# Kernel tuning notes

Hardware: AMD Instinct MI355X
Metric: run time of the kernel (lower is better)

Reference implementation:

```python
import jax, jax.numpy as jnp
import numpy as np

D_IN, D_BIAS, H, DH = 256, 128, 8, 32

def _layernorm(x, w, b, eps=1e-5):
    mu = jnp.mean(x, axis=-1, keepdims=True)
    var = jnp.var(x, axis=-1, keepdims=True)
    return (x - mu) * jax.lax.rsqrt(var + eps) * w + b

def setup_inputs() -> dict:
    key = jax.random.key(0)
    ks = jax.random.split(key, 8)
    B, L = 1, 768
    x = jax.random.normal(ks[0], (B, L, D_IN), dtype=jnp.float32)
    bias = jax.random.normal(ks[1], (B, L, L, D_BIAS), dtype=jnp.float32)
    s_in = 1.0 / np.sqrt(D_IN)
    s_b = 1.0 / np.sqrt(D_BIAS)
    return {
        "x": x,
        "bias": bias,
        "ln_in_w": jnp.ones((D_IN,), jnp.float32),
        "ln_in_b": jnp.zeros((D_IN,), jnp.float32),
        "ln_b_w": jnp.ones((D_BIAS,), jnp.float32),
        "ln_b_b": jnp.zeros((D_BIAS,), jnp.float32),
        "Wq": jax.random.normal(ks[2], (D_IN, H * DH), jnp.float32) * s_in,
        "Wk": jax.random.normal(ks[3], (D_IN, H * DH), jnp.float32) * s_in,
        "Wv": jax.random.normal(ks[4], (D_IN, H * DH), jnp.float32) * s_in,
        "Wb": jax.random.normal(ks[5], (D_BIAS, H), jnp.float32) * s_b,
        "Wg": jax.random.normal(ks[6], (D_IN, H * DH), jnp.float32) * 0.02,
        "bg": jnp.ones((H * DH,), jnp.float32),
        "Wo": jax.random.normal(ks[7], (H * DH, D_IN), jnp.float32) * 0.02,
        "bo": jnp.zeros((D_IN,), jnp.float32),
    }

def reference(x, bias, ln_in_w, ln_in_b, ln_b_w, ln_b_b, Wq, Wk, Wv, Wb, Wg, bg, Wo, bo):
    B, L, _ = x.shape
    scaling = 1.0 / np.sqrt(DH)
    xn = _layernorm(x, ln_in_w, ln_in_b)            # (B,L,D_IN)
    bn = _layernorm(bias, ln_b_w, ln_b_b)           # (B,L,L,D_BIAS)
    q = (xn @ Wq).reshape(B, L, H, DH)
    k = (xn @ Wk).reshape(B, L, H, DH) * scaling
    v = (xn @ Wv).reshape(B, L, H, DH)
    b = bn @ Wb                                     # (B,L,L,H)
    gate = jax.nn.sigmoid(xn @ Wg + bg)             # (B,L,H*DH)
    attn = jnp.einsum('bqhd,bkhd->bqkh', q, k) + b  # (B,q,k,h)
    attn = jax.nn.softmax(attn, axis=2)             # softmax over key dim
    out = jnp.einsum('bqkh,bkhd->bqhd', attn, v).reshape(B, L, H * DH)
    out = gate * out
    return out @ Wo + bo
```

## Files before the change

### kernel.cpp

```cpp
#include <hip/hip_runtime.h>

#define LQ 768
#define DIN 256
#define DB 128
#define NH 8
#define DH 32

#define OFF_QB 0
#define OFF_KT (LQ*DIN)
#define OFF_VB (2*LQ*DIN)
#define OFF_GB (3*LQ*DIN)
#define OFF_W2 (4*LQ*DIN)
#define OFF_SC (OFF_W2 + DB*NH)
#define OFF_LG (OFF_SC + 16)

__global__ __launch_bounds__(128) void setup_kernel(
    const float* __restrict__ lbw, const float* __restrict__ lbb,
    const float* __restrict__ Wb, float* __restrict__ W2, float* __restrict__ SC)
{
    const int d = threadIdx.x;
    const int lane = d & 63, wv = d >> 6;
    float w = lbw[d], b = lbb[d];
    float pS[NH], pC[NH];
    #pragma unroll
    for (int h = 0; h < NH; h++) {
        float wb = Wb[d*NH + h];
        float w2 = w * wb;
        W2[d*NH + h] = w2;
        pS[h] = w2;
        pC[h] = b * wb;
    }
    #pragma unroll
    for (int m = 1; m <= 32; m <<= 1) {
        #pragma unroll
        for (int h = 0; h < NH; h++) { pS[h] += __shfl_xor(pS[h], m); pC[h] += __shfl_xor(pC[h], m); }
    }
    __shared__ float red[2][16];
    if (lane == 0) {
        #pragma unroll
        for (int h = 0; h < NH; h++) { red[wv][h] = pS[h]; red[wv][NH+h] = pC[h]; }
    }
    __syncthreads();
    if (d < 16) SC[d] = red[0][d] + red[1][d];
}

__global__ __launch_bounds__(256) void proj_kernel(
    const float* __restrict__ x, const float* __restrict__ lnw, const float* __restrict__ lnb,
    const float* __restrict__ Wq, const float* __restrict__ Wk, const float* __restrict__ Wv,
    const float* __restrict__ Wg, const float* __restrict__ bg,
    float* __restrict__ qb, float* __restrict__ kT, float* __restrict__ vb, float* __restrict__ gb)
{
    const int tid = threadIdx.x;
    const int lane = tid & 63, rr = tid >> 6;
    const int row = blockIdx.x * 4 + rr;
    __shared__ float xn[4][DIN];

    float4 xv = ((const float4*)x)[row * (DIN/4) + lane];
    float s  = xv.x + xv.y + xv.z + xv.w;
    float ss = xv.x*xv.x + xv.y*xv.y + xv.z*xv.z + xv.w*xv.w;
    #pragma unroll
    for (int m = 1; m <= 32; m <<= 1) { s += __shfl_xor(s, m); ss += __shfl_xor(ss, m); }
    float mu  = s * (1.0f/DIN);
    float inv = rsqrtf(ss * (1.0f/DIN) - mu*mu + 1e-5f);
    float4 wv4 = ((const float4*)lnw)[lane];
    float4 bv4 = ((const float4*)lnb)[lane];
    float4 r4;
    r4.x = (xv.x - mu)*inv*wv4.x + bv4.x;
    r4.y = (xv.y - mu)*inv*wv4.y + bv4.y;
    r4.z = (xv.z - mu)*inv*wv4.z + bv4.z;
    r4.w = (xv.w - mu)*inv*wv4.w + bv4.w;
    *((float4*)&xn[rr][lane*4]) = r4;
    __syncthreads();

    const int col = tid;
    float aq[4] = {0,0,0,0}, ak[4] = {0,0,0,0}, av[4] = {0,0,0,0}, ag[4] = {0,0,0,0};
    for (int i4 = 0; i4 < DIN/4; i4++) {
        float4 x0 = *((const float4*)&xn[0][i4*4]);
        float4 x1 = *((const float4*)&xn[1][i4*4]);
        float4 x2 = *((const float4*)&xn[2][i4*4]);
        float4 x3 = *((const float4*)&xn[3][i4*4]);
        const float* p0 = (const float*)&x0;
        const float* p1 = (const float*)&x1;
        const float* p2 = (const float*)&x2;
        const float* p3 = (const float*)&x3;
        #pragma unroll
        for (int e = 0; e < 4; e++) {
            const int i = i4*4 + e;
            float wq = Wq[i*DIN + col], wk = Wk[i*DIN + col];
            float wvv = Wv[i*DIN + col], wg = Wg[i*DIN + col];
            aq[0] = fmaf(p0[e], wq, aq[0]); aq[1] = fmaf(p1[e], wq, aq[1]);
            aq[2] = fmaf(p2[e], wq, aq[2]); aq[3] = fmaf(p3[e], wq, aq[3]);
            ak[0] = fmaf(p0[e], wk, ak[0]); ak[1] = fmaf(p1[e], wk, ak[1]);
            ak[2] = fmaf(p2[e], wk, ak[2]); ak[3] = fmaf(p3[e], wk, ak[3]);
            av[0] = fmaf(p0[e], wvv, av[0]); av[1] = fmaf(p1[e], wvv, av[1]);
            av[2] = fmaf(p2[e], wvv, av[2]); av[3] = fmaf(p3[e], wvv, av[3]);
            ag[0] = fmaf(p0[e], wg, ag[0]); ag[1] = fmaf(p1[e], wg, ag[1]);
            ag[2] = fmaf(p2[e], wg, ag[2]); ag[3] = fmaf(p3[e], wg, ag[3]);
        }
    }
    const float kscale = 0.17677669529663687f;
    float bgv = bg[col];
    #pragma unroll
    for (int r = 0; r < 4; r++) {
        const int orow = blockIdx.x*4 + r;
        qb[orow*DIN + col] = aq[r];
        vb[orow*DIN + col] = av[r];
        gb[orow*DIN + col] = 1.0f/(1.0f + __expf(-(ag[r] + bgv)));
    }
    *((float4*)&kT[col*LQ + blockIdx.x*4]) =
        make_float4(ak[0]*kscale, ak[1]*kscale, ak[2]*kscale, ak[3]*kscale);
}

__global__ __launch_bounds__(128) void bias_kernel(
    const float* __restrict__ bias, const float* __restrict__ W2g,
    const float* __restrict__ SCg, float* __restrict__ logits)
{
    __shared__ float tile[2][64 * 129];
    const int tid  = threadIdx.x;
    const int w    = tid >> 6;
    const int lane = tid & 63;
    const int wid  = blockIdx.x * 2 + w;

    float* tw = &tile[w][0];
    const int wbase = (lane >> 5) * 129 + (lane & 31) * 4;
    const int rbase = lane * 129;

    float Sh[NH], Ch[NH];
    #pragma unroll
    for (int h = 0; h < NH; h++) { Sh[h] = SCg[h]; Ch[h] = SCg[NH + h]; }

    float4 v[32];

    const int tau0 = wid * 9;

    {
        const int q  = tau0 / 12;
        const int kb = (tau0 % 12) * 64;
        const float4* gs = (const float4*)(bias + ((size_t)q * LQ + kb) * DB);
        #pragma unroll
        for (int c = 0; c < 32; c++) v[c] = gs[c * 64 + lane];
        #pragma unroll
        for (int c = 0; c < 32; c++) {
            tw[wbase + c*258 + 0] = v[c].x;
            tw[wbase + c*258 + 1] = v[c].y;
            tw[wbase + c*258 + 2] = v[c].z;
            tw[wbase + c*258 + 3] = v[c].w;
        }
    }

    for (int t = 0; t < 9; t++) {
        const int tau = tau0 + t;

        if (t + 1 < 9) {
            const int qn  = (tau + 1) / 12;
            const int kbn = ((tau + 1) % 12) * 64;
            const float4* gs = (const float4*)(bias + ((size_t)qn * LQ + kbn) * DB);
            #pragma unroll
            for (int c = 0; c < 32; c++) v[c] = gs[c * 64 + lane];
        }
        asm volatile("" ::: "memory");

        float s = 0.f, ss = 0.f;
        float acc[NH] = {0,0,0,0,0,0,0,0};
        #pragma unroll 4
        for (int d = 0; d < DB; d++) {
            float xv = tw[rbase + d];
            const float* wr = W2g + d * NH;
            s += xv; ss = fmaf(xv, xv, ss);
            #pragma unroll
            for (int h = 0; h < NH; h++) acc[h] = fmaf(xv, wr[h], acc[h]);
        }

        {
            const int q  = tau / 12;
            const int kb = (tau % 12) * 64;
            float mu  = s * (1.0f/DB);
            float inv = rsqrtf(ss * (1.0f/DB) - mu*mu + 1e-5f);
            float lo[NH];
            #pragma unroll
            for (int h = 0; h < NH; h++)
                lo[h] = fmaf(inv, fmaf(-mu, Sh[h], acc[h]), Ch[h]);
            float4* dst = (float4*)(logits + ((size_t)q*LQ + kb + lane)*NH);
            dst[0] = make_float4(lo[0], lo[1], lo[2], lo[3]);
            dst[1] = make_float4(lo[4], lo[5], lo[6], lo[7]);
        }

        if (t + 1 < 9) {
            #pragma unroll
            for (int c = 0; c < 32; c++) {
                tw[wbase + c*258 + 0] = v[c].x;
                tw[wbase + c*258 + 1] = v[c].y;
                tw[wbase + c*258 + 2] = v[c].z;
                tw[wbase + c*258 + 3] = v[c].w;
            }
        }
    }
}

__global__ __launch_bounds__(256) void attn_kernel(
    const float* __restrict__ logits, const float* __restrict__ qbuf,
    const float* __restrict__ kT, const float* __restrict__ vbuf,
    const float* __restrict__ gb, const float* __restrict__ Wo,
    const float* __restrict__ bo, float* __restrict__ out)
{
    const int tid = threadIdx.x;
    const int q0 = blockIdx.x * 2;
    __shared__ float pT[2][NH][776];
    __shared__ float ao[2][DIN];
    __shared__ float isum[2][NH];

    #pragma unroll
    for (int r = 0; r < 2; r++) {
        const float4* rp = (const float4*)(logits + (size_t)(q0 + r)*LQ*NH);
        #pragma unroll
        for (int ii = 0; ii < 6; ii++) {
            int jj = ii*256 + tid;
            float4 t = rp[jj];
            int k = jj >> 1, h0 = (jj & 1) << 2;
            pT[r][h0+0][k] = t.x; pT[r][h0+1][k] = t.y;
            pT[r][h0+2][k] = t.z; pT[r][h0+3][k] = t.w;
        }
    }
    __syncthreads();

    if (tid < 192) {
        const float* q0p = qbuf + (size_t)q0*DIN;
        const float* q1p = q0p + DIN;
        #pragma unroll
        for (int h = 0; h < NH; h++) {
            float a00=0,a01=0,a02=0,a03=0, a10=0,a11=0,a12=0,a13=0;
            #pragma unroll
            for (int dd = 0; dd < DH; dd++) {
                const int d = h*DH + dd;
                float4 kv = *(const float4*)(kT + (size_t)d*LQ + tid*4);
                float qa = q0p[d], qc = q1p[d];
                a00 = fmaf(qa, kv.x, a00); a01 = fmaf(qa, kv.y, a01);
                a02 = fmaf(qa, kv.z, a02); a03 = fmaf(qa, kv.w, a03);
                a10 = fmaf(qc, kv.x, a10); a11 = fmaf(qc, kv.y, a11);
                a12 = fmaf(qc, kv.z, a12); a13 = fmaf(qc, kv.w, a13);
            }
            float4 p0 = *(float4*)&pT[0][h][tid*4];
            p0.x += a00; p0.y += a01; p0.z += a02; p0.w += a03;
            *(float4*)&pT[0][h][tid*4] = p0;
            float4 p1 = *(float4*)&pT[1][h][tid*4];
            p1.x += a10; p1.y += a11; p1.z += a12; p1.w += a13;
            *(float4*)&pT[1][h][tid*4] = p1;
        }
    }
    __syncthreads();

    {
        const int r = tid >> 7, h = (tid >> 4) & 7, l = tid & 15;
        float4* row = (float4*)&pT[r][h][0];
        float m = -1e30f;
        for (int i = l; i < 192; i += 16) {
            float4 v = row[i];
            m = fmaxf(m, fmaxf(fmaxf(v.x, v.y), fmaxf(v.z, v.w)));
        }
        #pragma unroll
        for (int mm = 1; mm <= 8; mm <<= 1) m = fmaxf(m, __shfl_xor(m, mm));
        float sum = 0.f;
        for (int i = l; i < 192; i += 16) {
            float4 v = row[i];
            v.x = __expf(v.x - m); v.y = __expf(v.y - m);
            v.z = __expf(v.z - m); v.w = __expf(v.w - m);
            sum += v.x + v.y + v.z + v.w;
            row[i] = v;
        }
        #pragma unroll
        for (int mm = 1; mm <= 8; mm <<= 1) sum += __shfl_xor(sum, mm);
        if (l == 0) isum[r][h] = 1.0f / sum;
    }
    __syncthreads();

    {
        const int h = tid >> 5, d = tid & 31;
        const float* vp = vbuf + h*DH + d;
        const float4* p0r = (const float4*)&pT[0][h][0];
        const float4* p1r = (const float4*)&pT[1][h][0];
        float a0 = 0.f, a1 = 0.f;
        for (int k4 = 0; k4 < 192; k4++) {
            float4 p0 = p0r[k4], p1 = p1r[k4];
            float v0 = vp[(size_t)(k4*4+0)*DIN];
            float v1 = vp[(size_t)(k4*4+1)*DIN];
            float v2 = vp[(size_t)(k4*4+2)*DIN];
            float v3 = vp[(size_t)(k4*4+3)*DIN];
            a0 = fmaf(p0.x, v0, a0); a0 = fmaf(p0.y, v1, a0);
            a0 = fmaf(p0.z, v2, a0); a0 = fmaf(p0.w, v3, a0);
            a1 = fmaf(p1.x, v0, a1); a1 = fmaf(p1.y, v1, a1);
            a1 = fmaf(p1.z, v2, a1); a1 = fmaf(p1.w, v3, a1);
        }
        ao[0][tid] = a0 * isum[0][h] * gb[(q0+0)*DIN + tid];
        ao[1][tid] = a1 * isum[1][h] * gb[(q0+1)*DIN + tid];
    }
    __syncthreads();

    {
        const int col = tid;
        float o0 = bo[col], o1 = o0;
        for (int i = 0; i < DIN; i++) {
            float wv = Wo[i*DIN + col];
            o0 = fmaf(ao[0][i], wv, o0);
            o1 = fmaf(ao[1][i], wv, o1);
        }
        out[(q0+0)*DIN + col] = o0;
        out[(q0+1)*DIN + col] = o1;
    }
}

extern "C" void kernel_launch(void* const* d_in, const int* in_sizes, int n_in,
                              void* d_out, int out_size, void* d_ws, size_t ws_size,
                              hipStream_t stream) {
    const float* x    = (const float*)d_in[0];
    const float* bias = (const float*)d_in[1];
    const float* lnw  = (const float*)d_in[2];
    const float* lnb  = (const float*)d_in[3];
    const float* lbw  = (const float*)d_in[4];
    const float* lbb  = (const float*)d_in[5];
    const float* Wq   = (const float*)d_in[6];
    const float* Wk   = (const float*)d_in[7];
    const float* Wv   = (const float*)d_in[8];
    const float* Wb   = (const float*)d_in[9];
    const float* Wg   = (const float*)d_in[10];
    const float* bg   = (const float*)d_in[11];
    const float* Wo   = (const float*)d_in[12];
    const float* bo   = (const float*)d_in[13];

    float* ws = (float*)d_ws;
    float* qb = ws + OFF_QB;
    float* kT = ws + OFF_KT;
    float* vb = ws + OFF_VB;
    float* gb = ws + OFF_GB;
    float* W2 = ws + OFF_W2;
    float* SC = ws + OFF_SC;
    float* lg = ws + OFF_LG;

    setup_kernel<<<1, 128, 0, stream>>>(lbw, lbb, Wb, W2, SC);
    proj_kernel<<<LQ/4, 256, 0, stream>>>(x, lnw, lnb, Wq, Wk, Wv, Wg, bg, qb, kT, vb, gb);
    bias_kernel<<<512, 128, 0, stream>>>(bias, W2, SC, lg);
    attn_kernel<<<LQ/2, 256, 0, stream>>>(lg, qb, kT, vb, gb, Wo, bo, (float*)d_out);
}
```

Baseline: 164.0 us.

## Precompute QK scores in a tiled kernel and fuse them into the bias-logit pass

Moves the per-head Q·K dot products out of the attention kernel into a separate shared-memory tiled qk kernel that writes a full L×L×H score buffer. The bias kernel is rewritten to one thread per (q,key) pair, reading the bias row directly instead of staging it through an LDS transpose, and adds the precomputed scores into the logits. The setup kernel is merged into the projection launch as an extra block, and K is stored row-major instead of transposed. In exchange this adds an extra ~19MB write and read of the QK buffer, and each thread's strided 512-byte bias reads may coalesce less well.

```diff
diff --git a/kernel.cpp b/kernel.cpp
--- a/kernel.cpp
+++ b/kernel.cpp
@@ -7,50 +7,53 @@
 #define DH 32
 
 #define OFF_QB 0
-#define OFF_KT (LQ*DIN)
+#define OFF_KB (LQ*DIN)
 #define OFF_VB (2*LQ*DIN)
 #define OFF_GB (3*LQ*DIN)
 #define OFF_W2 (4*LQ*DIN)
 #define OFF_SC (OFF_W2 + DB*NH)
-#define OFF_LG (OFF_SC + 16)
-
-__global__ __launch_bounds__(128) void setup_kernel(
-    const float* __restrict__ lbw, const float* __restrict__ lbb,
-    const float* __restrict__ Wb, float* __restrict__ W2, float* __restrict__ SC)
-{
-    const int d = threadIdx.x;
-    const int lane = d & 63, wv = d >> 6;
-    float w = lbw[d], b = lbb[d];
-    float pS[NH], pC[NH];
-    #pragma unroll
-    for (int h = 0; h < NH; h++) {
-        float wb = Wb[d*NH + h];
-        float w2 = w * wb;
-        W2[d*NH + h] = w2;
-        pS[h] = w2;
-        pC[h] = b * wb;
-    }
-    #pragma unroll
-    for (int m = 1; m <= 32; m <<= 1) {
-        #pragma unroll
-        for (int h = 0; h < NH; h++) { pS[h] += __shfl_xor(pS[h], m); pC[h] += __shfl_xor(pC[h], m); }
-    }
-    __shared__ float red[2][16];
-    if (lane == 0) {
-        #pragma unroll
-        for (int h = 0; h < NH; h++) { red[wv][h] = pS[h]; red[wv][NH+h] = pC[h]; }
-    }
-    __syncthreads();
-    if (d < 16) SC[d] = red[0][d] + red[1][d];
-}
-
-__global__ __launch_bounds__(256) void proj_kernel(
+#define OFF_QK (OFF_SC + 16)
+#define OFF_LG (OFF_QK + LQ*LQ*NH)
+
+__global__ __launch_bounds__(256) void projsetup_kernel(
     const float* __restrict__ x, const float* __restrict__ lnw, const float* __restrict__ lnb,
     const float* __restrict__ Wq, const float* __restrict__ Wk, const float* __restrict__ Wv,
     const float* __restrict__ Wg, const float* __restrict__ bg,
-    float* __restrict__ qb, float* __restrict__ kT, float* __restrict__ vb, float* __restrict__ gb)
+    const float* __restrict__ lbw, const float* __restrict__ lbb, const float* __restrict__ Wb,
+    float* __restrict__ qb, float* __restrict__ kb, float* __restrict__ vb, float* __restrict__ gb,
+    float* __restrict__ W2, float* __restrict__ SC)
 {
     const int tid = threadIdx.x;
+
+    if (blockIdx.x == 192) {
+        if (tid < 128) {
+            const int d = tid, lane = d & 63, wv = d >> 6;
+            float w = lbw[d], b = lbb[d];
+            float pS[NH], pC[NH];
+            #pragma unroll
+            for (int h = 0; h < NH; h++) {
+                float wb = Wb[d*NH + h];
+                float w2 = w * wb;
+                W2[d*NH + h] = w2;
+                pS[h] = w2;
+                pC[h] = b * wb;
+            }
+            #pragma unroll
+            for (int m = 1; m <= 32; m <<= 1) {
+                #pragma unroll
+                for (int h = 0; h < NH; h++) { pS[h] += __shfl_xor(pS[h], m); pC[h] += __shfl_xor(pC[h], m); }
+            }
+            __shared__ float red[2][16];
+            if (lane == 0) {
+                #pragma unroll
+                for (int h = 0; h < NH; h++) { red[wv][h] = pS[h]; red[wv][NH+h] = pC[h]; }
+            }
+            __syncthreads();
+            if (d < 16) SC[d] = red[0][d] + red[1][d];
+        }
+        return;
+    }
+
     const int lane = tid & 63, rr = tid >> 6;
     const int row = blockIdx.x * 4 + rr;
     __shared__ float xn[4][DIN];
@@ -104,102 +107,139 @@
     for (int r = 0; r < 4; r++) {
         const int orow = blockIdx.x*4 + r;
         qb[orow*DIN + col] = aq[r];
+        kb[orow*DIN + col] = ak[r] * kscale;
         vb[orow*DIN + col] = av[r];
         gb[orow*DIN + col] = 1.0f/(1.0f + __expf(-(ag[r] + bgv)));
     }
-    *((float4*)&kT[col*LQ + blockIdx.x*4]) =
-        make_float4(ak[0]*kscale, ak[1]*kscale, ak[2]*kscale, ak[3]*kscale);
-}
-
-__global__ __launch_bounds__(128) void bias_kernel(
+}
+
+__global__ __launch_bounds__(256) void qk_kernel(
+    const float* __restrict__ qb, const float* __restrict__ kb, float* __restrict__ qkT)
+{
+    __shared__ float q_l[32*260];
+    __shared__ float k_l[32*260];
+    const int tid = threadIdx.x;
+    const int bq = blockIdx.x, bk = blockIdx.y;
+
+    {
+        const int row = tid >> 3, cg = tid & 7;
+        const float4* qs = (const float4*)(qb + (size_t)(bq*32 + row)*DIN + cg*32);
+        const float4* ks = (const float4*)(kb + (size_t)(bk*32 + row)*DIN + cg*32);
+        #pragma unroll
+        for (int j = 0; j < 8; j++) {
+            *(float4*)&q_l[row*260 + cg*32 + j*4] = qs[j];
+            *(float4*)&k_l[row*260 + cg*32 + j*4] = ks[j];
+        }
+    }
+    __syncthreads();
+
+    const int tx = tid & 15, ty = tid >> 4;
+    float acc[2][2][NH];
+    #pragma unroll
+    for (int a = 0; a < 2; a++)
+        #pragma unroll
+        for (int b = 0; b < 2; b++)
+            #pragma unroll
+            for (int h = 0; h < NH; h++) acc[a][b][h] = 0.f;
+
+    #pragma unroll
+    for (int d4 = 0; d4 < 64; d4++) {
+        const int h = d4 >> 3;
+        float4 q0 = *(const float4*)&q_l[(ty*2+0)*260 + d4*4];
+        float4 q1 = *(const float4*)&q_l[(ty*2+1)*260 + d4*4];
+        float4 k0 = *(const float4*)&k_l[(tx*2+0)*260 + d4*4];
+        float4 k1 = *(const float4*)&k_l[(tx*2+1)*260 + d4*4];
+        acc[0][0][h] = fmaf(q0.x,k0.x,acc[0][0][h]); acc[0][0][h] = fmaf(q0.y,k0.y,acc[0][0][h]);
+        acc[0][0][h] = fmaf(q0.z,k0.z,acc[0][0][h]); acc[0][0][h] = fmaf(q0.w,k0.w,acc[0][0][h]);
+        acc[0][1][h] = fmaf(q0.x,k1.x,acc[0][1][h]); acc[0][1][h] = fmaf(q0.y,k1.y,acc[0][1][h]);
+        acc[0][1][h] = fmaf(q0.z,k1.z,acc[0][1][h]); acc[0][1][h] = fmaf(q0.w,k1.w,acc[0][1][h]);
+        acc[1][0][h] = fmaf(q1.x,k0.x,acc[1][0][h]); acc[1][0][h] = fmaf(q1.y,k0.y,acc[1][0][h]);
+        acc[1][0][h] = fmaf(q1.z,k0.z,acc[1][0][h]); acc[1][0][h] = fmaf(q1.w,k0.w,acc[1][0][h]);
+        acc[1][1][h] = fmaf(q1.x,k1.x,acc[1][1][h]); acc[1][1][h] = fmaf(q1.y,k1.y,acc[1][1][h]);
+        acc[1][1][h] = fmaf(q1.z,k1.z,acc[1][1][h]); acc[1][1][h] = fmaf(q1.w,k1.w,acc[1][1][h]);
+    }
+
+    #pragma unroll
+    for (int a = 0; a < 2; a++)
+        #pragma unroll
+        for (int b = 0; b < 2; b++) {
+            size_t base = ((size_t)(bq*32 + ty*2 + a)*LQ + (bk*32 + tx*2 + b))*NH;
+            *(float4*)(qkT + base)     = make_float4(acc[a][b][0], acc[a][b][1], acc[a][b][2], acc[a][b][3]);
+            *(float4*)(qkT + base + 4) = make_float4(acc[a][b][4], acc[a][b][5], acc[a][b][6], acc[a][b][7]);
+        }
+}
+
+__global__ __launch_bounds__(256, 6) void bias1t_kernel(
     const float* __restrict__ bias, const float* __restrict__ W2g,
-    const float* __restrict__ SCg, float* __restrict__ logits)
+    const float* __restrict__ SCg, const float* __restrict__ qkT,
+    float* __restrict__ logits)
 {
-    __shared__ float tile[2][64 * 129];
-    const int tid  = threadIdx.x;
-    const int w    = tid >> 6;
-    const int lane = tid & 63;
-    const int wid  = blockIdx.x * 2 + w;
-
-    float* tw = &tile[w][0];
-    const int wbase = (lane >> 5) * 129 + (lane & 31) * 4;
-    const int rbase = lane * 129;
-
-    float Sh[NH], Ch[NH];
-    #pragma unroll
-    for (int h = 0; h < NH; h++) { Sh[h] = SCg[h]; Ch[h] = SCg[NH + h]; }
-
-    float4 v[32];
-
-    const int tau0 = wid * 9;
-
-    {
-        const int q  = tau0 / 12;
-        const int kb = (tau0 % 12) * 64;
-        const float4* gs = (const float4*)(bias + ((size_t)q * LQ + kb) * DB);
-        #pragma unroll
-        for (int c = 0; c < 32; c++) v[c] = gs[c * 64 + lane];
-        #pragma unroll
-        for (int c = 0; c < 32; c++) {
-            tw[wbase + c*258 + 0] = v[c].x;
-            tw[wbase + c*258 + 1] = v[c].y;
-            tw[wbase + c*258 + 2] = v[c].z;
-            tw[wbase + c*258 + 3] = v[c].w;
-        }
-    }
-
-    for (int t = 0; t < 9; t++) {
-        const int tau = tau0 + t;
-
-        if (t + 1 < 9) {
-            const int qn  = (tau + 1) / 12;
-            const int kbn = ((tau + 1) % 12) * 64;
-            const float4* gs = (const float4*)(bias + ((size_t)qn * LQ + kbn) * DB);
-            #pragma unroll
-            for (int c = 0; c < 32; c++) v[c] = gs[c * 64 + lane];
-        }
-        asm volatile("" ::: "memory");
-
-        float s = 0.f, ss = 0.f;
-        float acc[NH] = {0,0,0,0,0,0,0,0};
-        #pragma unroll 4
-        for (int d = 0; d < DB; d++) {
-            float xv = tw[rbase + d];
-            const float* wr = W2g + d * NH;
+    const int bid = blockIdx.x;
+    const int q   = bid / 3;
+    const int key = (bid - q*3) * 256 + threadIdx.x;
+    const size_t off = (size_t)q * LQ + key;
+
+    const float4* src = (const float4*)(bias + off * DB);
+    const float4* qkp = (const float4*)(qkT + off * NH);
+    float4 qka = qkp[0];
+    float4 qkb = qkp[1];
+
+    float s = 0.f, ss = 0.f;
+    float acc[NH] = {0,0,0,0,0,0,0,0};
+
+    #pragma unroll
+    for (int c = 0; c < 8; c++) {
+        float4 b0 = src[c*4+0];
+        float4 b1 = src[c*4+1];
+        float4 b2 = src[c*4+2];
+        float4 b3 = src[c*4+3];
+        const float* wr = W2g + c*16*NH;
+        #pragma unroll
+        for (int e = 0; e < 4; e++) {
+            float xv = (&b0.x)[e];
             s += xv; ss = fmaf(xv, xv, ss);
             #pragma unroll
-            for (int h = 0; h < NH; h++) acc[h] = fmaf(xv, wr[h], acc[h]);
-        }
-
-        {
-            const int q  = tau / 12;
-            const int kb = (tau % 12) * 64;
-            float mu  = s * (1.0f/DB);
-            float inv = rsqrtf(ss * (1.0f/DB) - mu*mu + 1e-5f);
-            float lo[NH];
-            #pragma unroll
-            for (int h = 0; h < NH; h++)
-                lo[h] = fmaf(inv, fmaf(-mu, Sh[h], acc[h]), Ch[h]);
-            float4* dst = (float4*)(logits + ((size_t)q*LQ + kb + lane)*NH);
-            dst[0] = make_float4(lo[0], lo[1], lo[2], lo[3]);
-            dst[1] = make_float4(lo[4], lo[5], lo[6], lo[7]);
-        }
-
-        if (t + 1 < 9) {
-            #pragma unroll
-            for (int c = 0; c < 32; c++) {
-                tw[wbase + c*258 + 0] = v[c].x;
-                tw[wbase + c*258 + 1] = v[c].y;
-                tw[wbase + c*258 + 2] = v[c].z;
-                tw[wbase + c*258 + 3] = v[c].w;
-            }
-        }
-    }
+            for (int h = 0; h < NH; h++) acc[h] = fmaf(xv, wr[e*NH+h], acc[h]);
+        }
+        #pragma unroll
+        for (int e = 0; e < 4; e++) {
+            float xv = (&b1.x)[e];
+            s += xv; ss = fmaf(xv, xv, ss);
+            #pragma unroll
+            for (int h = 0; h < NH; h++) acc[h] = fmaf(xv, wr[(4+e)*NH+h], acc[h]);
+        }
+        #pragma unroll
+        for (int e = 0; e < 4; e++) {
+            float xv = (&b2.x)[e];
+            s += xv; ss = fmaf(xv, xv, ss);
+            #pragma unroll
+            for (int h = 0; h < NH; h++) acc[h] = fmaf(xv, wr[(8+e)*NH+h], acc[h]);
+        }
+        #pragma unroll
+        for (int e = 0; e < 4; e++) {
+            float xv = (&b3.x)[e];
+            s += xv; ss = fmaf(xv, xv, ss);
+            #pragma unroll
+            for (int h = 0; h < NH; h++) acc[h] = fmaf(xv, wr[(12+e)*NH+h], acc[h]);
+        }
+    }
+
+    float mu  = s * (1.0f/DB);
+    float inv = rsqrtf(ss * (1.0f/DB) - mu*mu + 1e-5f);
+    float lo[NH];
+    #pragma unroll
+    for (int h = 0; h < NH; h++)
+        lo[h] = fmaf(inv, fmaf(-mu, SCg[h], acc[h]), SCg[NH+h]);
+    lo[0] += qka.x; lo[1] += qka.y; lo[2] += qka.z; lo[3] += qka.w;
+    lo[4] += qkb.x; lo[5] += qkb.y; lo[6] += qkb.z; lo[7] += qkb.w;
+
+    float4* dst = (float4*)(logits + off * NH);
+    dst[0] = make_float4(lo[0], lo[1], lo[2], lo[3]);
+    dst[1] = make_float4(lo[4], lo[5], lo[6], lo[7]);
 }
 
 __global__ __launch_bounds__(256) void attn_kernel(
-    const float* __restrict__ logits, const float* __restrict__ qbuf,
-    const float* __restrict__ kT, const float* __restrict__ vbuf,
+    const float* __restrict__ logits, const float* __restrict__ vbuf,
     const float* __restrict__ gb, const float* __restrict__ Wo,
     const float* __restrict__ bo, float* __restrict__ out)
 {
@@ -219,32 +259,6 @@
             int k = jj >> 1, h0 = (jj & 1) << 2;
             pT[r][h0+0][k] = t.x; pT[r][h0+1][k] = t.y;
             pT[r][h0+2][k] = t.z; pT[r][h0+3][k] = t.w;
-        }
-    }
-    __syncthreads();
-
-    if (tid < 192) {
-        const float* q0p = qbuf + (size_t)q0*DIN;
-        const float* q1p = q0p + DIN;
-        #pragma unroll
-        for (int h = 0; h < NH; h++) {
-            float a00=0,a01=0,a02=0,a03=0, a10=0,a11=0,a12=0,a13=0;
-            #pragma unroll
-            for (int dd = 0; dd < DH; dd++) {
-                const int d = h*DH + dd;
-                float4 kv = *(const float4*)(kT + (size_t)d*LQ + tid*4);
-                float qa = q0p[d], qc = q1p[d];
-                a00 = fmaf(qa, kv.x, a00); a01 = fmaf(qa, kv.y, a01);
-                a02 = fmaf(qa, kv.z, a02); a03 = fmaf(qa, kv.w, a03);
-                a10 = fmaf(qc, kv.x, a10); a11 = fmaf(qc, kv.y, a11);
-                a12 = fmaf(qc, kv.z, a12); a13 = fmaf(qc, kv.w, a13);
-            }
-            float4 p0 = *(float4*)&pT[0][h][tid*4];
-            p0.x += a00; p0.y += a01; p0.z += a02; p0.w += a03;
-            *(float4*)&pT[0][h][tid*4] = p0;
-            float4 p1 = *(float4*)&pT[1][h][tid*4];
-            p1.x += a10; p1.y += a11; p1.z += a12; p1.w += a13;
-            *(float4*)&pT[1][h][tid*4] = p1;
         }
     }
     __syncthreads();
@@ -328,15 +342,17 @@
 
     float* ws = (float*)d_ws;
     float* qb = ws + OFF_QB;
-    float* kT = ws + OFF_KT;
+    float* kb = ws + OFF_KB;
     float* vb = ws + OFF_VB;
     float* gb = ws + OFF_GB;
     float* W2 = ws + OFF_W2;
     float* SC = ws + OFF_SC;
+    float* qk = ws + OFF_QK;
     float* lg = ws + OFF_LG;
 
-    setup_kernel<<<1, 128, 0, stream>>>(lbw, lbb, Wb, W2, SC);
-    proj_kernel<<<LQ/4, 256, 0, stream>>>(x, lnw, lnb, Wq, Wk, Wv, Wg, bg, qb, kT, vb, gb);
-    bias_kernel<<<512, 128, 0, stream>>>(bias, W2, SC, lg);
-    attn_kernel<<<LQ/2, 256, 0, stream>>>(lg, qb, kT, vb, gb, Wo, bo, (float*)d_out);
-}
+    projsetup_kernel<<<193, 256, 0, stream>>>(x, lnw, lnb, Wq, Wk, Wv, Wg, bg,
+                                              lbw, lbb, Wb, qb, kb, vb, gb, W2, SC);
+    qk_kernel<<<dim3(24, 24), 256, 0, stream>>>(qb, kb, qk);
+    bias1t_kernel<<<2304, 256, 0, stream>>>(bias, W2, SC, qk, lg);
+    attn_kernel<<<LQ/2, 256, 0, stream>>>(lg, vb, gb, Wo, bo, (float*)d_out);
+}
```

Result: slower. 198.9 us (+21.3%).

## Stream bias tiles via direct global-to-LDS loads and merge setup into projection kernel

Applied to the files above, without the earlier changes.

Rewrites the pair-bias layernorm-projection kernel to use global_load_lds (direct DMA into shared memory) with a 4-stage ring of swizzled 16-byte chunks and explicit vmcnt waits. This replaces the register-staged load and transpose store, so the bias stream can run ahead of compute with less VGPR pressure. The grid moves from 512 to 1536 blocks, each covering 384 keys of one query row. Separately, the tiny setup kernel becomes an extra block of the projection kernel to save a launch. The risk is correctness of the hand-tuned waitcnt counts and the LDS swizzle.

```diff
diff --git a/kernel.cpp b/kernel.cpp
--- a/kernel.cpp
+++ b/kernel.cpp
@@ -14,43 +14,52 @@
 #define OFF_SC (OFF_W2 + DB*NH)
 #define OFF_LG (OFF_SC + 16)
 
-__global__ __launch_bounds__(128) void setup_kernel(
-    const float* __restrict__ lbw, const float* __restrict__ lbb,
-    const float* __restrict__ Wb, float* __restrict__ W2, float* __restrict__ SC)
-{
-    const int d = threadIdx.x;
-    const int lane = d & 63, wv = d >> 6;
-    float w = lbw[d], b = lbb[d];
-    float pS[NH], pC[NH];
-    #pragma unroll
-    for (int h = 0; h < NH; h++) {
-        float wb = Wb[d*NH + h];
-        float w2 = w * wb;
-        W2[d*NH + h] = w2;
-        pS[h] = w2;
-        pC[h] = b * wb;
-    }
-    #pragma unroll
-    for (int m = 1; m <= 32; m <<= 1) {
-        #pragma unroll
-        for (int h = 0; h < NH; h++) { pS[h] += __shfl_xor(pS[h], m); pC[h] += __shfl_xor(pC[h], m); }
-    }
-    __shared__ float red[2][16];
-    if (lane == 0) {
-        #pragma unroll
-        for (int h = 0; h < NH; h++) { red[wv][h] = pS[h]; red[wv][NH+h] = pC[h]; }
-    }
-    __syncthreads();
-    if (d < 16) SC[d] = red[0][d] + red[1][d];
-}
-
-__global__ __launch_bounds__(256) void proj_kernel(
+__device__ __forceinline__ void gload_lds16(const void* g, void* l) {
+    __builtin_amdgcn_global_load_lds(
+        (__attribute__((address_space(1))) const void*)g,
+        (__attribute__((address_space(3))) void*)l,
+        16, 0, 0);
+}
+
+__global__ __launch_bounds__(256) void projsetup_kernel(
     const float* __restrict__ x, const float* __restrict__ lnw, const float* __restrict__ lnb,
     const float* __restrict__ Wq, const float* __restrict__ Wk, const float* __restrict__ Wv,
     const float* __restrict__ Wg, const float* __restrict__ bg,
-    float* __restrict__ qb, float* __restrict__ kT, float* __restrict__ vb, float* __restrict__ gb)
+    const float* __restrict__ lbw, const float* __restrict__ lbb, const float* __restrict__ Wb,
+    float* __restrict__ qb, float* __restrict__ kT, float* __restrict__ vb, float* __restrict__ gb,
+    float* __restrict__ W2, float* __restrict__ SC)
 {
     const int tid = threadIdx.x;
+
+    if (blockIdx.x == 192) {
+        if (tid < 128) {
+            const int d = tid, lane = d & 63, wv = d >> 6;
+            float w = lbw[d], b = lbb[d];
+            float pS[NH], pC[NH];
+            #pragma unroll
+            for (int h = 0; h < NH; h++) {
+                float wb = Wb[d*NH + h];
+                float w2 = w * wb;
+                W2[d*NH + h] = w2;
+                pS[h] = w2;
+                pC[h] = b * wb;
+            }
+            #pragma unroll
+            for (int m = 1; m <= 32; m <<= 1) {
+                #pragma unroll
+                for (int h = 0; h < NH; h++) { pS[h] += __shfl_xor(pS[h], m); pC[h] += __shfl_xor(pC[h], m); }
+            }
+            __shared__ float red[2][16];
+            if (lane == 0) {
+                #pragma unroll
+                for (int h = 0; h < NH; h++) { red[wv][h] = pS[h]; red[wv][NH+h] = pC[h]; }
+            }
+            __syncthreads();
+            if (d < 16) SC[d] = red[0][d] + red[1][d];
+        }
+        return;
+    }
+
     const int lane = tid & 63, rr = tid >> 6;
     const int row = blockIdx.x * 4 + rr;
     __shared__ float xn[4][DIN];
@@ -111,89 +120,86 @@
         make_float4(ak[0]*kscale, ak[1]*kscale, ak[2]*kscale, ak[3]*kscale);
 }
 
-__global__ __launch_bounds__(128) void bias_kernel(
+__global__ __launch_bounds__(128) void bias13_kernel(
     const float* __restrict__ bias, const float* __restrict__ W2g,
     const float* __restrict__ SCg, float* __restrict__ logits)
 {
-    __shared__ float tile[2][64 * 129];
+    __shared__ float tiles[2][4][1024];
     const int tid  = threadIdx.x;
     const int w    = tid >> 6;
     const int lane = tid & 63;
-    const int wid  = blockIdx.x * 2 + w;
-
-    float* tw = &tile[w][0];
-    const int wbase = (lane >> 5) * 129 + (lane & 31) * 4;
-    const int rbase = lane * 129;
+    const int q    = blockIdx.y;
+    const int keybase = blockIdx.x * 384 + w * 192;
+
+    const char* gq = (const char*)bias + ((size_t)q*LQ + keybase) * (DB*4);
+    char* const lb0 = (char*)&tiles[w][0][0];
+
+    const int keyc = lane >> 2;
+    const int rot  = ((lane & 3) - ((lane >> 3) & 3)) & 3;
+    const int soff = keyc*512 + rot*16;
+
+    #define STAGE(T) {                                                       \
+        const char* gt = gq + ((T) >> 3)*32768 + ((T) & 7)*64;               \
+        char* lb = lb0 + (((T) & 3) << 12);                                  \
+        _Pragma("unroll")                                                    \
+        for (int c = 0; c < 4; c++)                                          \
+            gload_lds16(gt + c*8192 + soff, lb + c*1024);                    \
+    }
+
+    STAGE(0); STAGE(1); STAGE(2); STAGE(3);
 
     float Sh[NH], Ch[NH];
     #pragma unroll
     for (int h = 0; h < NH; h++) { Sh[h] = SCg[h]; Ch[h] = SCg[NH + h]; }
 
-    float4 v[32];
-
-    const int tau0 = wid * 9;
-
-    {
-        const int q  = tau0 / 12;
-        const int kb = (tau0 % 12) * 64;
-        const float4* gs = (const float4*)(bias + ((size_t)q * LQ + kb) * DB);
-        #pragma unroll
-        for (int c = 0; c < 32; c++) v[c] = gs[c * 64 + lane];
-        #pragma unroll
-        for (int c = 0; c < 32; c++) {
-            tw[wbase + c*258 + 0] = v[c].x;
-            tw[wbase + c*258 + 1] = v[c].y;
-            tw[wbase + c*258 + 2] = v[c].z;
-            tw[wbase + c*258 + 3] = v[c].w;
-        }
-    }
-
-    for (int t = 0; t < 9; t++) {
-        const int tau = tau0 + t;
-
-        if (t + 1 < 9) {
-            const int qn  = (tau + 1) / 12;
-            const int kbn = ((tau + 1) % 12) * 64;
-            const float4* gs = (const float4*)(bias + ((size_t)qn * LQ + kbn) * DB);
-            #pragma unroll
-            for (int c = 0; c < 32; c++) v[c] = gs[c * 64 + lane];
-        }
-        asm volatile("" ::: "memory");
-
+    const int a0 = lane * 64;
+    const int rl = (lane >> 1) & 3;
+
+    float lo[3][NH];
+
+    #pragma unroll
+    for (int kb = 0; kb < 3; kb++) {
         float s = 0.f, ss = 0.f;
         float acc[NH] = {0,0,0,0,0,0,0,0};
-        #pragma unroll 4
-        for (int d = 0; d < DB; d++) {
-            float xv = tw[rbase + d];
-            const float* wr = W2g + d * NH;
-            s += xv; ss = fmaf(xv, xv, ss);
+        #pragma unroll 1
+        for (int sd = 0; sd < 8; sd++) {
+            const int T = kb*8 + sd;
+            if (T <= 20)      asm volatile("s_waitcnt vmcnt(12)" ::: "memory");
+            else if (T == 21) asm volatile("s_waitcnt vmcnt(8)"  ::: "memory");
+            else if (T == 22) asm volatile("s_waitcnt vmcnt(4)"  ::: "memory");
+            else              asm volatile("s_waitcnt vmcnt(0)"  ::: "memory");
+
+            const char* tb = lb0 + ((T & 3) << 12);
+            const float* wr0 = W2g + sd*16*NH;
             #pragma unroll
-            for (int h = 0; h < NH; h++) acc[h] = fmaf(xv, wr[h], acc[h]);
-        }
-
-        {
-            const int q  = tau / 12;
-            const int kb = (tau % 12) * 64;
-            float mu  = s * (1.0f/DB);
-            float inv = rsqrtf(ss * (1.0f/DB) - mu*mu + 1e-5f);
-            float lo[NH];
-            #pragma unroll
-            for (int h = 0; h < NH; h++)
-                lo[h] = fmaf(inv, fmaf(-mu, Sh[h], acc[h]), Ch[h]);
-            float4* dst = (float4*)(logits + ((size_t)q*LQ + kb + lane)*NH);
-            dst[0] = make_float4(lo[0], lo[1], lo[2], lo[3]);
-            dst[1] = make_float4(lo[4], lo[5], lo[6], lo[7]);
-        }
-
-        if (t + 1 < 9) {
-            #pragma unroll
-            for (int c = 0; c < 32; c++) {
-                tw[wbase + c*258 + 0] = v[c].x;
-                tw[wbase + c*258 + 1] = v[c].y;
-                tw[wbase + c*258 + 2] = v[c].z;
-                tw[wbase + c*258 + 3] = v[c].w;
-            }
-        }
+            for (int j = 0; j < 4; j++) {
+                float4 bv = *(const float4*)(tb + a0 + (((rl + j) & 3) << 4));
+                const float* wr = wr0 + j*4*NH;
+                #pragma unroll
+                for (int e = 0; e < 4; e++) {
+                    float xv = (&bv.x)[e];
+                    s += xv; ss = fmaf(xv, xv, ss);
+                    #pragma unroll
+                    for (int h = 0; h < NH; h++)
+                        acc[h] = fmaf(xv, wr[e*NH + h], acc[h]);
+                }
+            }
+            asm volatile("s_waitcnt lgkmcnt(0)" ::: "memory");
+            if (T + 4 < 24) STAGE(T + 4);
+        }
+        float mu  = s * (1.0f/DB);
+        float inv = rsqrtf(ss * (1.0f/DB) - mu*mu + 1e-5f);
+        #pragma unroll
+        for (int h = 0; h < NH; h++)
+            lo[kb][h] = fmaf(inv, fmaf(-mu, Sh[h], acc[h]), Ch[h]);
+    }
+    #undef STAGE
+
+    #pragma unroll
+    for (int kb = 0; kb < 3; kb++) {
+        float4* dst = (float4*)(logits + ((size_t)q*LQ + keybase + kb*64 + lane)*NH);
+        dst[0] = make_float4(lo[kb][0], lo[kb][1], lo[kb][2], lo[kb][3]);
+        dst[1] = make_float4(lo[kb][4], lo[kb][5], lo[kb][6], lo[kb][7]);
     }
 }
 
@@ -335,8 +341,8 @@
     float* SC = ws + OFF_SC;
     float* lg = ws + OFF_LG;
 
-    setup_kernel<<<1, 128, 0, stream>>>(lbw, lbb, Wb, W2, SC);
-    proj_kernel<<<LQ/4, 256, 0, stream>>>(x, lnw, lnb, Wq, Wk, Wv, Wg, bg, qb, kT, vb, gb);
-    bias_kernel<<<512, 128, 0, stream>>>(bias, W2, SC, lg);
+    projsetup_kernel<<<193, 256, 0, stream>>>(x, lnw, lnb, Wq, Wk, Wv, Wg, bg,
+                                              lbw, lbb, Wb, qb, kT, vb, gb, W2, SC);
+    bias13_kernel<<<dim3(2, LQ), 128, 0, stream>>>(bias, W2, SC, lg);
     attn_kernel<<<LQ/2, 256, 0, stream>>>(lg, qb, kT, vb, gb, Wo, bo, (float*)d_out);
 }
```

After: 155.7 us, median of 2. -5.0%, faster.
